# Optimization experiments

Measured on AMD Instinct MI355X. Metric: run time of the kernel, lower is better.

Reference implementation:

```python
import jax, jax.numpy as jnp
import numpy as np


def setup_inputs() -> dict:
    key = jax.random.key(0)
    z = jax.random.normal(key, (8, 4096, 1024), dtype=jnp.float32)
    return {"z": z}


def reference(z):
    d = z.shape[-1]
    # sort descending along last dim
    z_sorted = -jnp.sort(-z, axis=-1)
    z_cumsum = jnp.cumsum(z_sorted, axis=-1)
    k = jnp.arange(1, d + 1, dtype=z.dtype)  # [d]
    rhs = 1 + k * z_sorted
    is_gt = (rhs > z_cumsum).astype(z.dtype)
    # largest k satisfying the support condition
    k_z = jnp.max(is_gt * k, axis=-1, keepdims=True)  # [..., 1]
    idx = k_z.astype(jnp.int32) - 1
    z_cumsum_k = jnp.take_along_axis(z_cumsum, idx, axis=-1)
    tau = (z_cumsum_k - 1) / k_z
    p = jnp.clip(z - tau, 0.0, None)
    return p
```

## Files before the change

kernel.cpp:

```cpp
#include <hip/hip_runtime.h>


#define ROW_D 1024

typedef float f4 __attribute__((ext_vector_type(4)));

template <int CTRL, int RMASK>
__device__ __forceinline__ float dpp_mv(float x) {
    return __builtin_bit_cast(float, __builtin_amdgcn_update_dpp(
        __builtin_bit_cast(int, x), __builtin_bit_cast(int, x),
        CTRL, RMASK, 0xf, false));
}

__device__ __forceinline__ float dpp_sum_to63(float x) {
    x += dpp_mv<0x111, 0xf>(x);
    x += dpp_mv<0x112, 0xf>(x);
    x += dpp_mv<0x114, 0xf>(x);
    x += dpp_mv<0x118, 0xf>(x);
    x += dpp_mv<0x142, 0xa>(x);
    x += dpp_mv<0x143, 0xc>(x);
    return x;
}
__device__ __forceinline__ float dpp_max_to63(float x) {
    x = fmaxf(x, dpp_mv<0x111, 0xf>(x));
    x = fmaxf(x, dpp_mv<0x112, 0xf>(x));
    x = fmaxf(x, dpp_mv<0x114, 0xf>(x));
    x = fmaxf(x, dpp_mv<0x118, 0xf>(x));
    x = fmaxf(x, dpp_mv<0x142, 0xa>(x));
    x = fmaxf(x, dpp_mv<0x143, 0xc>(x));
    return x;
}
__device__ __forceinline__ float bcast63(float x) {
    return __builtin_bit_cast(float,
        __builtin_amdgcn_readlane(__builtin_bit_cast(int, x), 63));
}

__global__ __launch_bounds__(256) void sparsemax_kernel(
    const float* __restrict__ z, float* __restrict__ out, int nrows) {
    const int lane = (int)(threadIdx.x & 63u);
    const int row  = (int)(blockIdx.x << 2) + (int)(threadIdx.x >> 6);
    if (row >= nrows) return;

    const f4* __restrict__ zin = reinterpret_cast<const f4*>(z + (size_t)row * ROW_D);
    f4* __restrict__ pout      = reinterpret_cast<f4*>(out + (size_t)row * ROW_D);

    f4 v[4];
#pragma unroll
    for (int j = 0; j < 4; ++j) v[j] = zin[lane + 64 * j];

    float mj[4];
#pragma unroll
    for (int j = 0; j < 4; ++j)
        mj[j] = fmaxf(fmaxf(v[j].x, v[j].y), fmaxf(v[j].z, v[j].w));
    float m = fmaxf(fmaxf(mj[0], mj[1]), fmaxf(mj[2], mj[3]));
    m = bcast63(dpp_max_to63(m));

    float t = m - 1.0f;
#pragma unroll 1
    for (int it = 0; it < 16; ++it) {
        float sj[4];
        int n = 0;
#pragma unroll
        for (int j = 0; j < 4; ++j) {
            const float d0 = v[j].x - t, d1 = v[j].y - t;
            const float d2 = v[j].z - t, d3 = v[j].w - t;
            sj[j] = (fmaxf(d0, 0.0f) + fmaxf(d1, 0.0f)) +
                    (fmaxf(d2, 0.0f) + fmaxf(d3, 0.0f));
            n += __popcll(__ballot(d0 > 0.0f));
            n += __popcll(__ballot(d1 > 0.0f));
            n += __popcll(__ballot(d2 > 0.0f));
            n += __popcll(__ballot(d3 > 0.0f));
        }
        float S = bcast63(dpp_sum_to63((sj[0] + sj[1]) + (sj[2] + sj[3])));
        const float t2 = t + (S - 1.0f) / (float)n;
        if (t2 - t <= 1e-6f) { t = t2; break; }
        t = t2;
    }

#pragma unroll
    for (int j = 0; j < 4; ++j) {
        f4 o;
        o.x = fmaxf(v[j].x - t, 0.0f);
        o.y = fmaxf(v[j].y - t, 0.0f);
        o.z = fmaxf(v[j].z - t, 0.0f);
        o.w = fmaxf(v[j].w - t, 0.0f);
        __builtin_nontemporal_store(o, pout + lane + 64 * j);
    }
}

extern "C" void kernel_launch(void* const* d_in, const int* in_sizes, int n_in,
                              void* d_out, int out_size, void* d_ws, size_t ws_size,
                              hipStream_t stream) {
    const float* z = (const float*)d_in[0];
    float* out = (float*)d_out;
    const int n = in_sizes[0];
    const int nrows = n / ROW_D;
    const int blocks = (nrows + 3) / 4;
    sparsemax_kernel<<<blocks, 256, 0, stream>>>(z, out, nrows);
}
```

Baseline: 229.1 us.

## Compact candidates above max-1 per lane before Newton iterations for tau

Before iterating, each lane keeps up to three of its elements that exceed max-1, since only those can lie in the support. If no lane holds more than three, the Newton iterations run on these three registers instead of all sixteen elements per lane, which cuts the ALU and ballot work per iteration. Otherwise it falls back to the full loop, whose iteration cap rises from 16 to 24. The cost is an extra select pass and a divergent branch.

```diff
diff --git a/kernel.cpp b/kernel.cpp
--- a/kernel.cpp
+++ b/kernel.cpp
@@ -2,6 +2,7 @@
 
 
 #define ROW_D 1024
+#define NEG_PAD -3.0e38f
 
 typedef float f4 __attribute__((ext_vector_type(4)));
 
@@ -11,7 +12,6 @@
         __builtin_bit_cast(int, x), __builtin_bit_cast(int, x),
         CTRL, RMASK, 0xf, false));
 }
-
 __device__ __forceinline__ float dpp_sum_to63(float x) {
     x += dpp_mv<0x111, 0xf>(x);
     x += dpp_mv<0x112, 0xf>(x);
@@ -54,27 +54,58 @@
         mj[j] = fmaxf(fmaxf(v[j].x, v[j].y), fmaxf(v[j].z, v[j].w));
     float m = fmaxf(fmaxf(mj[0], mj[1]), fmaxf(mj[2], mj[3]));
     m = bcast63(dpp_max_to63(m));
+    const float lo0 = m - 1.0f;
 
-    float t = m - 1.0f;
+    float c0 = NEG_PAD, c1 = NEG_PAD, c2 = NEG_PAD;
+    int cnt = 0;
+#pragma unroll
+    for (int j = 0; j < 4; ++j) {
+        const float e[4] = {v[j].x, v[j].y, v[j].z, v[j].w};
+#pragma unroll
+        for (int c = 0; c < 4; ++c) {
+            const bool g = e[c] > lo0;
+            c2 = g ? c1 : c2;
+            c1 = g ? c0 : c1;
+            c0 = g ? e[c] : c0;
+            cnt += g ? 1 : 0;
+        }
+    }
+
+    float t = lo0;
+    if (__ballot(cnt > 3) == 0ULL) {
 #pragma unroll 1
-    for (int it = 0; it < 16; ++it) {
-        float sj[4];
-        int n = 0;
-#pragma unroll
-        for (int j = 0; j < 4; ++j) {
-            const float d0 = v[j].x - t, d1 = v[j].y - t;
-            const float d2 = v[j].z - t, d3 = v[j].w - t;
-            sj[j] = (fmaxf(d0, 0.0f) + fmaxf(d1, 0.0f)) +
-                    (fmaxf(d2, 0.0f) + fmaxf(d3, 0.0f));
-            n += __popcll(__ballot(d0 > 0.0f));
+        for (int it = 0; it < 16; ++it) {
+            const float d0 = c0 - t, d1 = c1 - t, d2 = c2 - t;
+            const float s = fmaxf(d0, 0.0f) + (fmaxf(d1, 0.0f) + fmaxf(d2, 0.0f));
+            int n = __popcll(__ballot(d0 > 0.0f));
             n += __popcll(__ballot(d1 > 0.0f));
             n += __popcll(__ballot(d2 > 0.0f));
-            n += __popcll(__ballot(d3 > 0.0f));
+            const float S = bcast63(dpp_sum_to63(s));
+            const float t2 = t + (S - 1.0f) / (float)n;
+            if (t2 - t <= 1e-6f) { t = t2; break; }
+            t = t2;
         }
-        float S = bcast63(dpp_sum_to63((sj[0] + sj[1]) + (sj[2] + sj[3])));
-        const float t2 = t + (S - 1.0f) / (float)n;
-        if (t2 - t <= 1e-6f) { t = t2; break; }
-        t = t2;
+    } else {
+#pragma unroll 1
+        for (int it = 0; it < 24; ++it) {
+            float sj[4];
+            int n = 0;
+#pragma unroll
+            for (int j = 0; j < 4; ++j) {
+                const float d0 = v[j].x - t, d1 = v[j].y - t;
+                const float d2 = v[j].z - t, d3 = v[j].w - t;
+                sj[j] = (fmaxf(d0, 0.0f) + fmaxf(d1, 0.0f)) +
+                        (fmaxf(d2, 0.0f) + fmaxf(d3, 0.0f));
+                n += __popcll(__ballot(d0 > 0.0f));
+                n += __popcll(__ballot(d1 > 0.0f));
+                n += __popcll(__ballot(d2 > 0.0f));
+                n += __popcll(__ballot(d3 > 0.0f));
+            }
+            const float S = bcast63(dpp_sum_to63((sj[0] + sj[1]) + (sj[2] + sj[3])));
+            const float t2 = t + (S - 1.0f) / (float)n;
+            if (t2 - t <= 1e-6f) { t = t2; break; }
+            t = t2;
+        }
     }
 
 #pragma unroll
```

After: 229.4 us. About the same (+0.1%).
